# Optimization experiments

Measured on AMD Instinct MI355X. Metric: run time of the kernel, lower is better.

The kernel has to match this reference:

```python
import math
import jax, jax.numpy as jnp
import numpy as np

B, S, D = 8, 2048, 512
D_MODEL = 512

def setup_inputs() -> dict:
    key = jax.random.key(0)
    kq, kk, kv = jax.random.split(key, 3)
    return {
        "query": jax.random.normal(kq, (B, S, D), dtype=jnp.float32),
        "key":   jax.random.normal(kk, (B, S, D), dtype=jnp.float32),
        "value": jax.random.normal(kv, (B, S, D), dtype=jnp.float32),
    }

def reference(query, key, value):
    # scores: [B, S, S]
    scores = jnp.einsum("bqd,bkd->bqk", query, key) / math.sqrt(D_MODEL)
    k = max(1, int(scores.shape[-1] * 0.1))
    top_scores, top_idx = jax.lax.top_k(scores, k)  # [B, S, k]
    # scatter top-k scores into a zero matrix (non-topk entries stay 0,
    # and DO participate in the softmax, matching the torch code)
    b_idx = jnp.arange(scores.shape[0])[:, None, None]
    q_idx = jnp.arange(scores.shape[1])[None, :, None]
    sparse = jnp.zeros_like(scores).at[b_idx, q_idx, top_idx].set(top_scores)
    attn = jax.nn.softmax(sparse, axis=-1)
    return jnp.einsum("bqk,bkd->bqd", attn, value)
```

## Files before the change

### kernel.cpp

```cpp
#include <hip/hip_runtime.h>
#include <math.h>

#define B_ 8
#define S_ 2048
#define D_ 512
#define KTOP 204
#define QK_SCALE 0.044194173824159216f

typedef short bfrag8 __attribute__((ext_vector_type(8)));
typedef float facc4 __attribute__((ext_vector_type(4)));

__device__ __forceinline__ unsigned short f2bf(float f) {
  unsigned u = __float_as_uint(f);
  u += 0x7FFFu + ((u >> 16) & 1);
  return (unsigned short)(u >> 16);
}

__device__ __forceinline__ unsigned fkey(float f) {
  unsigned b = __float_as_uint(f);
  return (b & 0x80000000u) ? ~b : (b | 0x80000000u);
}
__device__ __forceinline__ float keyfloat(unsigned k) {
  unsigned b = (k & 0x80000000u) ? (k & 0x7FFFFFFFu) : ~k;
  return __uint_as_float(b);
}

__device__ __forceinline__ void load16(const unsigned short* g, unsigned short* l) {
  __builtin_amdgcn_global_load_lds(
      (const __attribute__((address_space(1))) void*)g,
      (__attribute__((address_space(3))) void*)l, 16, 0, 0);
}

__global__ __launch_bounds__(256) void prep(const float* __restrict__ Q,
                                            const float* __restrict__ K,
                                            const float* __restrict__ V,
                                            unsigned short* __restrict__ Qb,
                                            unsigned short* __restrict__ Kb,
                                            unsigned short* __restrict__ VT) {
  __shared__ float tile[32][33];
  const unsigned b = blockIdx.x;
  if (b < 16384u) {
    const float* in = (b < 8192u) ? Q : K;
    unsigned short* out = (b < 8192u) ? Qb : Kb;
    const int i = (int)((b & 8191u) * 1024u + threadIdx.x * 4u);
    float4 v = *(const float4*)(in + i);
    ushort4 o;
    o.x = f2bf(v.x); o.y = f2bf(v.y); o.z = f2bf(v.z); o.w = f2bf(v.w);
    *(ushort4*)(out + i) = o;
  } else {
    const unsigned t = b - 16384u;
    const int d0 = (int)(t & 15u) * 32;
    const int k0 = (int)((t >> 4) & 63u) * 32;
    const int bz = (int)(t >> 10);
    const float* Vb = V + (size_t)bz * S_ * D_;
    unsigned short* VTb = VT + (size_t)bz * D_ * S_;
    const int c = threadIdx.x & 31, r = threadIdx.x >> 5;
#pragma unroll
    for (int rr = 0; rr < 32; rr += 8)
      tile[r + rr][c] = Vb[(size_t)(k0 + r + rr) * D_ + d0 + c];
    __syncthreads();
#pragma unroll
    for (int rr = 0; rr < 32; rr += 8)
      VTb[(size_t)(d0 + r + rr) * S_ + k0 + c] = f2bf(tile[c][r + rr]);
  }
}


__device__ __forceinline__ void stage64(const unsigned short* M, int ld, int k0,
                                        int tid, unsigned short* dst) {
  const int wave = tid >> 6;
  const int row = tid >> 3;
  const int col = ((tid & 7) ^ (row & 7)) * 8;
  unsigned short* wdst = dst + wave * 512;
  const unsigned short* src = M + (size_t)row * ld + k0 + col;
#pragma unroll
  for (int s = 0; s < 4; ++s)
    load16(src + (size_t)(s * 32) * ld, wdst + s * 2048);
}

__device__ __forceinline__ void mfma_step64(const unsigned short* sA, const unsigned short* sB,
                                            int mrow, int nrow, int l15, int quad,
                                            facc4 (&acc)[4][4]) {
#pragma unroll
  for (int c = 0; c < 2; ++c) {
    const int slot = ((c * 4 + quad) ^ (l15 & 7)) * 8;
    bfrag8 af[4], bq[4];
#pragma unroll
    for (int i = 0; i < 4; ++i)
      af[i] = *(const bfrag8*)(sA + (mrow + 16 * i + l15) * 64 + slot);
#pragma unroll
    for (int j2 = 0; j2 < 4; ++j2)
      bq[j2] = *(const bfrag8*)(sB + (nrow + 16 * j2 + l15) * 64 + slot);
#pragma unroll
    for (int i = 0; i < 4; ++i)
#pragma unroll
      for (int j2 = 0; j2 < 4; ++j2)
        acc[i][j2] = __builtin_amdgcn_mfma_f32_16x16x32_bf16(af[i], bq[j2], acc[i][j2], 0, 0, 0);
  }
}

__global__ __launch_bounds__(256) void gemm_qk(
    const unsigned short* __restrict__ A, int lda, long long astr,
    const unsigned short* __restrict__ Bm, int ldb, long long bstr,
    float* __restrict__ C, int ldc, long long cstr,
    int kdim, float scale) {
  const unsigned j = blockIdx.x + 16u * blockIdx.y + 256u * blockIdx.z;
  const unsigned bz = j & 7u;
  const unsigned q = j >> 3;
  const unsigned by = q & 15u;
  const unsigned bx = q >> 4;

  __shared__ unsigned short smA[2][128 * 64];
  __shared__ unsigned short smB[2][128 * 64];
  const int tid = threadIdx.x;
  const int wave = tid >> 6, lane = tid & 63;
  const int quad = lane >> 4, l15 = lane & 15;
  const unsigned short* Ab = A + (long long)bz * astr + (size_t)(by * 128) * lda;
  const unsigned short* Bb = Bm + (long long)bz * bstr + (size_t)(bx * 128) * ldb;
  const int mrow = 64 * (wave >> 1);
  const int nrow = 64 * (wave & 1);

  facc4 acc[4][4];
  const facc4 fzero = {0.f, 0.f, 0.f, 0.f};
#pragma unroll
  for (int i = 0; i < 4; ++i)
#pragma unroll
    for (int j2 = 0; j2 < 4; ++j2) acc[i][j2] = fzero;

  stage64(Ab, lda, 0, tid, smA[0]);
  stage64(Bb, ldb, 0, tid, smB[0]);
  __syncthreads();

  for (int k0 = 0; k0 < kdim; k0 += 128) {
    stage64(Ab, lda, k0 + 64, tid, smA[1]);
    stage64(Bb, ldb, k0 + 64, tid, smB[1]);
    mfma_step64(smA[0], smB[0], mrow, nrow, l15, quad, acc);
    __syncthreads();
    if (k0 + 128 < kdim) {
      stage64(Ab, lda, k0 + 128, tid, smA[0]);
      stage64(Bb, ldb, k0 + 128, tid, smB[0]);
    }
    mfma_step64(smA[1], smB[1], mrow, nrow, l15, quad, acc);
    __syncthreads();
  }

  float* Cb = C + (long long)bz * cstr;
  const int mg = by * 128 + mrow;
  const int ng = bx * 128 + nrow;
#pragma unroll
  for (int i = 0; i < 4; ++i)
#pragma unroll
    for (int j2 = 0; j2 < 4; ++j2)
#pragma unroll
      for (int r = 0; r < 4; ++r)
        Cb[(size_t)(mg + 16 * i + quad * 4 + r) * ldc + ng + 16 * j2 + l15] = acc[i][j2][r] * scale;
}

__global__ __launch_bounds__(256) void gemm_pv(
    const unsigned short* __restrict__ A, int lda, long long astr,
    const unsigned short* __restrict__ Bm, int ldb, long long bstr,
    float* __restrict__ C, int ldc, long long cstr,
    int kdim, float scale) {
  const unsigned j = blockIdx.x + 4u * blockIdx.y + 64u * blockIdx.z;
  const unsigned bz = j & 7u;
  const unsigned q = j >> 3;
  const unsigned bx = q & 3u;
  const unsigned by = q >> 2;

  __shared__ unsigned short smA[2][128 * 64];
  __shared__ unsigned short smB[2][128 * 64];
  const int tid = threadIdx.x;
  const int wave = tid >> 6, lane = tid & 63;
  const int quad = lane >> 4, l15 = lane & 15;
  const unsigned short* Ab = A + (long long)bz * astr + (size_t)(by * 128) * lda;
  const unsigned short* Bb = Bm + (long long)bz * bstr + (size_t)(bx * 128) * ldb;
  const int mrow = 64 * (wave >> 1);
  const int nrow = 64 * (wave & 1);

  facc4 acc[4][4];
  const facc4 fzero = {0.f, 0.f, 0.f, 0.f};
#pragma unroll
  for (int i = 0; i < 4; ++i)
#pragma unroll
    for (int j2 = 0; j2 < 4; ++j2) acc[i][j2] = fzero;

  stage64(Ab, lda, 0, tid, smA[0]);
  stage64(Bb, ldb, 0, tid, smB[0]);
  __syncthreads();

  for (int k0 = 0; k0 < kdim; k0 += 128) {
    stage64(Ab, lda, k0 + 64, tid, smA[1]);
    stage64(Bb, ldb, k0 + 64, tid, smB[1]);
    mfma_step64(smA[0], smB[0], mrow, nrow, l15, quad, acc);
    __syncthreads();
    if (k0 + 128 < kdim) {
      stage64(Ab, lda, k0 + 128, tid, smA[0]);
      stage64(Bb, ldb, k0 + 128, tid, smB[0]);
    }
    mfma_step64(smA[1], smB[1], mrow, nrow, l15, quad, acc);
    __syncthreads();
  }

  float* Cb = C + (long long)bz * cstr;
  const int mg = by * 128 + mrow;
  const int ng = bx * 128 + nrow;
#pragma unroll
  for (int i = 0; i < 4; ++i)
#pragma unroll
    for (int j2 = 0; j2 < 4; ++j2)
#pragma unroll
      for (int r = 0; r < 4; ++r)
        Cb[(size_t)(mg + 16 * i + quad * 4 + r) * ldc + ng + 16 * j2 + l15] = acc[i][j2][r] * scale;
}

__device__ __forceinline__ unsigned sel256(const unsigned* bins, int lane,
                                           unsigned krem, unsigned* krem_out) {
  const uint4 b = *(const uint4*)(bins + lane * 4);
  const unsigned s = b.x + b.y + b.z + b.w;
  unsigned t = s;
#pragma unroll
  for (int off = 1; off < 64; off <<= 1) {
    unsigned u = (unsigned)__shfl_down((int)t, off);
    t += (lane + off < 64) ? u : 0u;
  }
  const unsigned texcl = t - s;
  const unsigned c3 = texcl + b.w;
  const unsigned c2 = c3 + b.z;
  const unsigned c1 = c2 + b.y;
  const unsigned c0 = c1 + b.x;
  unsigned pack = 0;
  if (c0 >= krem && c1 < krem)    pack = ((krem - c1) << 8) | (lane * 4 + 0);
  if (c1 >= krem && c2 < krem)    pack = ((krem - c2) << 8) | (lane * 4 + 1);
  if (c2 >= krem && c3 < krem)    pack = ((krem - c3) << 8) | (lane * 4 + 2);
  if (c3 >= krem && texcl < krem) pack = ((krem - texcl) << 8) | (lane * 4 + 3);
#pragma unroll
  for (int off = 1; off < 64; off <<= 1)
    pack |= (unsigned)__shfl_xor((int)pack, off);
  *krem_out = pack >> 8;
  return pack & 255u;
}

__global__ __launch_bounds__(256) void topk_softmax(float* __restrict__ scores) {
  __shared__ unsigned binsAll[2][256];
  __shared__ unsigned xchg[2][4];
  const int tid = threadIdx.x;
  const int wave = tid >> 6, lane = tid & 63;
  const int pair = wave >> 1, h = wave & 1;
  const long long row = (long long)blockIdx.x * 2 + pair;
  float* srow = scores + row * 2048 + h * 1024;
  unsigned* bins = binsAll[pair];
  unsigned* xch = xchg[pair];

  unsigned k[16];
#pragma unroll
  for (int c = 0; c < 2; ++c) {
    float4 a = *(const float4*)(srow + c * 512 + lane * 8);
    float4 b = *(const float4*)(srow + c * 512 + lane * 8 + 4);
    k[c * 8 + 0] = fkey(a.x); k[c * 8 + 1] = fkey(a.y);
    k[c * 8 + 2] = fkey(a.z); k[c * 8 + 3] = fkey(a.w);
    k[c * 8 + 4] = fkey(b.x); k[c * 8 + 5] = fkey(b.y);
    k[c * 8 + 6] = fkey(b.z); k[c * 8 + 7] = fkey(b.w);
  }

  {
    uint2 z; z.x = 0; z.y = 0;
    *(uint2*)(bins + (h * 64 + lane) * 2) = z;
  }
  unsigned kmax = 0;
#pragma unroll
  for (int i = 0; i < 16; ++i) kmax = max(kmax, k[i]);
#pragma unroll
  for (int off = 1; off < 64; off <<= 1)
    kmax = max(kmax, (unsigned)__shfl_xor((int)kmax, off));
  if (lane == 0) xch[h] = kmax;
  __syncthreads();
  kmax = max(xch[0], xch[1]);
  const float m = fmaxf(keyfloat(kmax), 0.f);

#pragma unroll
  for (int i = 0; i < 16; ++i) {
    const int t = (int)(k[i] >> 16) - 0xBF00;
    if (t >= 1) atomicAdd(&bins[min(t, 255)], 1u);
  }
  __syncthreads();
  if (h == 0) {
    unsigned kr;
    const unsigned d = sel256(bins, lane, KTOP, &kr);
    if (lane == 0) xch[2] = (kr << 8) | d;
    asm volatile("s_waitcnt lgkmcnt(0)" ::: "memory");
    uint4 z4; z4.x = 0; z4.y = 0; z4.z = 0; z4.w = 0;
    *(uint4*)(bins + lane * 4) = z4;
  }
  __syncthreads();
  unsigned pack = xch[2];
  const unsigned d1 = pack & 255u;
  unsigned krem = pack >> 8;

  const bool fb = (d1 < 1u || d1 > 254u);
  unsigned prefix, mmask;
  if (!fb) { prefix = (0xBF00u + d1) << 16; mmask = 0xFFFF0000u; }
  else     { prefix = 0u; mmask = 0u; krem = KTOP; }

  for (int s = 1; s <= 4; ++s) {
    const bool active = fb || (s <= 2);
    const int shift = fb ? (32 - 8 * s) : ((s == 1) ? 8 : 0);
    if (active) {
#pragma unroll
      for (int i = 0; i < 16; ++i)
        if ((k[i] & mmask) == prefix) atomicAdd(&bins[(k[i] >> shift) & 255u], 1u);
    }
    __syncthreads();
    if (h == 0 && active) {
      unsigned kr;
      const unsigned d = sel256(bins, lane, krem, &kr);
      if (lane == 0) xch[2] = (kr << 8) | d;
      asm volatile("s_waitcnt lgkmcnt(0)" ::: "memory");
      uint4 z4; z4.x = 0; z4.y = 0; z4.z = 0; z4.w = 0;
      *(uint4*)(bins + lane * 4) = z4;
    }
    __syncthreads();
    if (active) {
      pack = xch[2];
      prefix |= (pack & 255u) << shift;
      krem = pack >> 8;
      mmask |= 0xFFu << shift;
    }
  }
  const unsigned tkey = prefix;

  unsigned tiem = 0;
#pragma unroll
  for (int i = 0; i < 16; ++i)
    if (k[i] == tkey) tiem |= 1u << i;
  unsigned tc = (unsigned)__popc(tiem);
#pragma unroll
  for (int off = 1; off < 64; off <<= 1)
    tc += (unsigned)__shfl_xor((int)tc, off);
  if (h == 0 && lane == 0) xch[3] = tc;
  __syncthreads();
  const unsigned tcA = xch[3];
  const int whichHalf = (krem <= tcA) ? 0 : 1;
  if (h == whichHalf) {
    unsigned need = whichHalf ? (krem - tcA) : krem;
    unsigned cutl;
    for (;;) {
      unsigned myidx = 0xFFFFFFFFu;
      if (tiem) {
        int i = __ffs((int)tiem) - 1;
        myidx = (unsigned)(h * 1024) + ((unsigned)(i >> 3)) * 512u +
                (unsigned)lane * 8u + (unsigned)(i & 7);
      }
      unsigned minidx = myidx;
#pragma unroll
      for (int off = 1; off < 64; off <<= 1)
        minidx = min(minidx, (unsigned)__shfl_xor((int)minidx, off));
      if (--need == 0 || minidx == 0xFFFFFFFFu) { cutl = minidx; break; }
      if (myidx == minidx) tiem &= tiem - 1;
    }
    if (lane == 0) xch[2] = cutl;
  }
  __syncthreads();
  const unsigned cut = xch[2];

  const float eqw = __expf(keyfloat(tkey) - m);
  const float base = __expf(-m);
  float zsum = 0.f;
#pragma unroll
  for (int i = 0; i < 16; ++i) {
    const unsigned key = k[i];
    const unsigned idx = (unsigned)(h * 1024) + ((unsigned)(i >> 3)) * 512u +
                         (unsigned)lane * 8u + (unsigned)(i & 7);
    float w;
    if (key > tkey) w = __expf(keyfloat(key) - m);
    else w = (key == tkey && idx <= cut) ? eqw : base;
    zsum += w;
    k[i] = __float_as_uint(w);
  }
#pragma unroll
  for (int off = 1; off < 64; off <<= 1) zsum += __shfl_xor(zsum, off);
  if (lane == 0) xch[h] = __float_as_uint(zsum);
  __syncthreads();
  const float Z = __uint_as_float(xch[0]) + __uint_as_float(xch[1]);
  const float invZ = 1.f / Z;

  unsigned short* arow = (unsigned short*)scores + row * 4096 + h * 1024;
#pragma unroll
  for (int c = 0; c < 2; ++c) {
    union { unsigned short u[8]; int4 v4; } pk;
#pragma unroll
    for (int j = 0; j < 8; ++j)
      pk.u[j] = f2bf(__uint_as_float(k[c * 8 + j]) * invZ);
    *(int4*)(arow + c * 512 + lane * 8) = pk.v4;
  }
}

extern "C" void kernel_launch(void* const* d_in, const int* in_sizes, int n_in,
                              void* d_out, int out_size, void* d_ws, size_t ws_size,
                              hipStream_t stream) {
  const float* Q = (const float*)d_in[0];
  const float* K = (const float*)d_in[1];
  const float* V = (const float*)d_in[2];
  float* out = (float*)d_out;
  char* ws = (char*)d_ws;
  unsigned short* Qb = (unsigned short*)(ws);
  unsigned short* Kb = (unsigned short*)(ws + ((size_t)16 << 20));
  unsigned short* VT = (unsigned short*)(ws + ((size_t)32 << 20));
  float* scores = (float*)(ws + ((size_t)48 << 20));

  prep<<<24576, 256, 0, stream>>>(Q, K, V, Qb, Kb, VT);
  gemm_qk<<<dim3(S_ / 128, S_ / 128, B_), 256, 0, stream>>>(
      Qb, D_, (long long)S_ * D_, Kb, D_, (long long)S_ * D_,
      scores, S_, (long long)S_ * S_, D_, QK_SCALE);
  topk_softmax<<<B_ * S_ / 2, 256, 0, stream>>>(scores);
  gemm_pv<<<dim3(D_ / 128, S_ / 128, B_), 256, 0, stream>>>(
      (const unsigned short*)scores, 4096, (long long)S_ * 4096,
      VT, S_, (long long)D_ * S_, out, D_, (long long)S_ * D_, S_, 1.0f);
}
```

Baseline: 275.0 us.

## Replace QK GEMM with 256x256-tile 8-wave kernel using phased prefetch pipeline

Replaces the 128x128-tile, 4-wave QK^T GEMM with a 256x256-tile, 512-thread kernel. Each wave computes a 128x64 output block, and global-to-LDS staging is split into four half-tile phases interleaved with MFMA work. The phases use explicit vmcnt waits, barriers and setprio to overlap loads with compute. This raises data reuse per tile and hides load latency, at the cost of more registers and LDS (128KB per block), only 512 blocks, and fragile hand-written wait counts.

```diff
diff --git a/kernel.cpp b/kernel.cpp
--- a/kernel.cpp
+++ b/kernel.cpp
@@ -66,6 +66,132 @@
 }
 
 
+__device__ __forceinline__ void stage_half(const unsigned short* M, int ld, int k0,
+                                           int tid, unsigned short* dst) {
+  const int w = tid >> 6;
+  const int r = tid >> 3;
+  const int c = tid & 7;
+  const unsigned short* src = M + (size_t)r * ld + k0 + ((c ^ (r & 7)) * 8);
+  unsigned short* wdst = dst + w * 512;
+  load16(src, wdst);
+  load16(src + (size_t)64 * ld, wdst + 4096);
+}
+
+#define QK8_PHASE(MF0, ...)                                                    \
+  {                                                                            \
+    af[0][0] = *(const bfrag8*)(curA + aoff + (MF0) * 1024 + sl0);             \
+    af[0][1] = *(const bfrag8*)(curA + aoff + (MF0) * 1024 + sl1);             \
+    af[1][0] = *(const bfrag8*)(curA + aoff + ((MF0) + 1) * 1024 + sl0);       \
+    af[1][1] = *(const bfrag8*)(curA + aoff + ((MF0) + 1) * 1024 + sl1);       \
+    __VA_ARGS__;                                                               \
+    __builtin_amdgcn_s_barrier();                                              \
+    asm volatile("s_waitcnt lgkmcnt(0)" ::: "memory");                         \
+    __builtin_amdgcn_sched_barrier(0);                                         \
+    __builtin_amdgcn_s_setprio(1);                                             \
+    _Pragma("unroll")                                                          \
+    for (int kc = 0; kc < 2; ++kc) {                                           \
+      _Pragma("unroll")                                                        \
+      for (int mi = 0; mi < 2; ++mi) {                                         \
+        _Pragma("unroll")                                                      \
+        for (int nf = 0; nf < 4; ++nf)                                         \
+          acc[(MF0) + mi][nf] = __builtin_amdgcn_mfma_f32_16x16x32_bf16(       \
+              af[mi][kc], bf[nf][kc], acc[(MF0) + mi][nf], 0, 0, 0);           \
+      }                                                                        \
+    }                                                                          \
+    __builtin_amdgcn_s_setprio(0);                                             \
+  }
+
+__global__ __launch_bounds__(512) void gemm_qk8(
+    const unsigned short* __restrict__ A, int lda, long long astr,
+    const unsigned short* __restrict__ Bm, int ldb, long long bstr,
+    float* __restrict__ C, int ldc, long long cstr,
+    int kdim, float scale) {
+  const unsigned j = blockIdx.x + 8u * blockIdx.y + 64u * blockIdx.z;
+  const unsigned bz = j & 7u;
+  const unsigned q = j >> 3;
+  const unsigned by = q & 7u;
+  const unsigned bx = q >> 3;
+
+  __shared__ unsigned short smA[2][256 * 64];
+  __shared__ unsigned short smB[2][256 * 64];
+  const int tid = threadIdx.x;
+  const int wave = tid >> 6, lane = tid & 63;
+  const int wm = wave >> 2, wn = wave & 3;
+  const int quad = lane >> 4, l15 = lane & 15;
+  const unsigned short* Ab = A + (long long)bz * astr + (size_t)(by * 256) * lda;
+  const unsigned short* Bb = Bm + (long long)bz * bstr + (size_t)(bx * 256) * ldb;
+
+  const int aoff = (wm * 128 + l15) * 64;
+  const int boff = (wn * 64 + l15) * 64;
+  const int sl0 = ((quad) ^ (l15 & 7)) * 8;
+  const int sl1 = ((4 + quad) ^ (l15 & 7)) * 8;
+
+  facc4 acc[8][4];
+  const facc4 fzero = {0.f, 0.f, 0.f, 0.f};
+#pragma unroll
+  for (int mf = 0; mf < 8; ++mf)
+#pragma unroll
+    for (int nf = 0; nf < 4; ++nf) acc[mf][nf] = fzero;
+
+  const int T = kdim >> 6;
+
+  stage_half(Ab, lda, 0, tid, smA[0]);
+  stage_half(Ab + (size_t)128 * lda, lda, 0, tid, smA[0] + 8192);
+  stage_half(Bb, ldb, 0, tid, smB[0]);
+  stage_half(Bb + (size_t)128 * ldb, ldb, 0, tid, smB[0] + 8192);
+  stage_half(Bb, ldb, 64, tid, smB[1]);
+  stage_half(Bb + (size_t)128 * ldb, ldb, 64, tid, smB[1] + 8192);
+  asm volatile("s_waitcnt vmcnt(4)" ::: "memory");
+  __builtin_amdgcn_s_barrier();
+  __builtin_amdgcn_sched_barrier(0);
+
+  for (int t = 0; t < T; ++t) {
+    const unsigned short* curA = smA[t & 1];
+    const unsigned short* curB = smB[t & 1];
+    unsigned short* nA = smA[(t & 1) ^ 1];
+    unsigned short* nB = smB[t & 1];
+    bfrag8 bf[4][2];
+    bfrag8 af[2][2];
+
+#pragma unroll
+    for (int nf = 0; nf < 4; ++nf) {
+      bf[nf][0] = *(const bfrag8*)(curB + boff + nf * 1024 + sl0);
+      bf[nf][1] = *(const bfrag8*)(curB + boff + nf * 1024 + sl1);
+    }
+    QK8_PHASE(0, if (t + 1 < T) stage_half(Ab, lda, (t + 1) * 64, tid, nA));
+    __builtin_amdgcn_s_barrier();
+
+    QK8_PHASE(2, if (t + 1 < T)
+                   stage_half(Ab + (size_t)128 * lda, lda, (t + 1) * 64, tid, nA + 8192));
+    __builtin_amdgcn_s_barrier();
+
+    QK8_PHASE(4, if (t + 2 < T) stage_half(Bb, ldb, (t + 2) * 64, tid, nB));
+    __builtin_amdgcn_s_barrier();
+
+    QK8_PHASE(6, if (t + 2 < T)
+                   stage_half(Bb + (size_t)128 * ldb, ldb, (t + 2) * 64, tid, nB + 8192));
+    if (t < T - 2) {
+      asm volatile("s_waitcnt vmcnt(4)" ::: "memory");
+    } else {
+      asm volatile("s_waitcnt vmcnt(0)" ::: "memory");
+    }
+    __builtin_amdgcn_s_barrier();
+    __builtin_amdgcn_sched_barrier(0);
+  }
+
+  float* Cb = C + (long long)bz * cstr;
+  const int mg = by * 256 + wm * 128;
+  const int ng = bx * 256 + wn * 64;
+#pragma unroll
+  for (int mf = 0; mf < 8; ++mf)
+#pragma unroll
+    for (int nf = 0; nf < 4; ++nf)
+#pragma unroll
+      for (int r = 0; r < 4; ++r)
+        Cb[(size_t)(mg + mf * 16 + quad * 4 + r) * ldc + ng + nf * 16 + l15] =
+            acc[mf][nf][r] * scale;
+}
+
 __device__ __forceinline__ void stage64(const unsigned short* M, int ld, int k0,
                                         int tid, unsigned short* dst) {
   const int wave = tid >> 6;
@@ -97,63 +223,6 @@
       for (int j2 = 0; j2 < 4; ++j2)
         acc[i][j2] = __builtin_amdgcn_mfma_f32_16x16x32_bf16(af[i], bq[j2], acc[i][j2], 0, 0, 0);
   }
-}
-
-__global__ __launch_bounds__(256) void gemm_qk(
-    const unsigned short* __restrict__ A, int lda, long long astr,
-    const unsigned short* __restrict__ Bm, int ldb, long long bstr,
-    float* __restrict__ C, int ldc, long long cstr,
-    int kdim, float scale) {
-  const unsigned j = blockIdx.x + 16u * blockIdx.y + 256u * blockIdx.z;
-  const unsigned bz = j & 7u;
-  const unsigned q = j >> 3;
-  const unsigned by = q & 15u;
-  const unsigned bx = q >> 4;
-
-  __shared__ unsigned short smA[2][128 * 64];
-  __shared__ unsigned short smB[2][128 * 64];
-  const int tid = threadIdx.x;
-  const int wave = tid >> 6, lane = tid & 63;
-  const int quad = lane >> 4, l15 = lane & 15;
-  const unsigned short* Ab = A + (long long)bz * astr + (size_t)(by * 128) * lda;
-  const unsigned short* Bb = Bm + (long long)bz * bstr + (size_t)(bx * 128) * ldb;
-  const int mrow = 64 * (wave >> 1);
-  const int nrow = 64 * (wave & 1);
-
-  facc4 acc[4][4];
-  const facc4 fzero = {0.f, 0.f, 0.f, 0.f};
-#pragma unroll
-  for (int i = 0; i < 4; ++i)
-#pragma unroll
-    for (int j2 = 0; j2 < 4; ++j2) acc[i][j2] = fzero;
-
-  stage64(Ab, lda, 0, tid, smA[0]);
-  stage64(Bb, ldb, 0, tid, smB[0]);
-  __syncthreads();
-
-  for (int k0 = 0; k0 < kdim; k0 += 128) {
-    stage64(Ab, lda, k0 + 64, tid, smA[1]);
-    stage64(Bb, ldb, k0 + 64, tid, smB[1]);
-    mfma_step64(smA[0], smB[0], mrow, nrow, l15, quad, acc);
-    __syncthreads();
-    if (k0 + 128 < kdim) {
-      stage64(Ab, lda, k0 + 128, tid, smA[0]);
-      stage64(Bb, ldb, k0 + 128, tid, smB[0]);
-    }
-    mfma_step64(smA[1], smB[1], mrow, nrow, l15, quad, acc);
-    __syncthreads();
-  }
-
-  float* Cb = C + (long long)bz * cstr;
-  const int mg = by * 128 + mrow;
-  const int ng = bx * 128 + nrow;
-#pragma unroll
-  for (int i = 0; i < 4; ++i)
-#pragma unroll
-    for (int j2 = 0; j2 < 4; ++j2)
-#pragma unroll
-      for (int r = 0; r < 4; ++r)
-        Cb[(size_t)(mg + 16 * i + quad * 4 + r) * ldc + ng + 16 * j2 + l15] = acc[i][j2][r] * scale;
 }
 
 __global__ __launch_bounds__(256) void gemm_pv(
@@ -408,7 +477,7 @@
   float* scores = (float*)(ws + ((size_t)48 << 20));
 
   prep<<<24576, 256, 0, stream>>>(Q, K, V, Qb, Kb, VT);
-  gemm_qk<<<dim3(S_ / 128, S_ / 128, B_), 256, 0, stream>>>(
+  gemm_qk8<<<dim3(8, 8, 8), 512, 0, stream>>>(
       Qb, D_, (long long)S_ * D_, Kb, D_, (long long)S_ * D_,
       scores, S_, (long long)S_ * S_, D_, QK_SCALE);
   topk_softmax<<<B_ * S_ / 2, 256, 0, stream>>>(scores);
```

Measured after the change: 275.5 us. Within noise of the previous version (+0.2%).
